# Performance work log

Measured on AMD Instinct MI355X. Metric: run time of the kernel, lower is better.

The kernel has to match this reference:

```python
import jax, jax.numpy as jnp
import numpy as np

N = 50000
TOPK = 32
IN_C = 128
OUT_C = 64
NEG_SLOPE = 0.2
BN_EPS = 1e-5


def setup_inputs() -> dict:
    key = jax.random.key(0)
    ks = jax.random.split(key, 8)
    x = jax.random.normal(ks[0], (N, IN_C), dtype=jnp.float32)
    embedding = jax.random.normal(ks[1], (N, OUT_C), dtype=jnp.float32)
    # edges: each node has TOPK incoming edges, no self loops
    tgt = jnp.repeat(jnp.arange(N, dtype=jnp.int64), TOPK)
    off = jax.random.randint(ks[2], (N * TOPK,), 1, N, dtype=jnp.int64)
    src = (tgt + off) % N
    edge_index = jnp.stack([src, tgt], axis=0)
    lin_w = jax.random.normal(ks[3], (OUT_C, IN_C), dtype=jnp.float32) * (1.0 / np.sqrt(IN_C))
    att_i = jax.random.normal(ks[4], (1, 1, OUT_C), dtype=jnp.float32) * 0.1
    att_j = jax.random.normal(ks[5], (1, 1, OUT_C), dtype=jnp.float32) * 0.1
    att_em_i = jax.random.normal(ks[6], (1, 1, OUT_C), dtype=jnp.float32) * 0.1
    att_em_j = jax.random.normal(ks[7], (1, 1, OUT_C), dtype=jnp.float32) * 0.1
    bias = jnp.zeros((OUT_C,), dtype=jnp.float32)
    bn_gamma = jnp.ones((OUT_C,), dtype=jnp.float32)
    bn_beta = jnp.zeros((OUT_C,), dtype=jnp.float32)
    return {"x": x, "embedding": embedding, "edge_index": edge_index,
            "lin_w": lin_w, "att_i": att_i, "att_j": att_j,
            "att_em_i": att_em_i, "att_em_j": att_em_j, "bias": bias,
            "bn_gamma": bn_gamma, "bn_beta": bn_beta}


def _gnn_forward(x, embedding, lin_w, att_i, att_j, att_em_i, att_em_j,
                 bias, bn_gamma, bn_beta, src, tgt):
    n = x.shape[0]
    # linear transform: [N, heads=1, OUT_C]
    x_lin = (x @ lin_w.T).reshape(n, 1, OUT_C)
    # gather per edge (self loops already appended to src/tgt)
    x_i = x_lin[tgt]                      # [Etot, 1, C]
    x_j = x_lin[src]                      # [Etot, 1, C]
    emb_i = embedding[tgt][:, None, :]    # [Etot, 1, C]
    emb_j = embedding[src][:, None, :]
    # attention logits, eq (6)-(8)
    alpha = ((x_i * att_i).sum(-1) + (emb_i * att_em_i).sum(-1)
             + (x_j * att_j).sum(-1) + (emb_j * att_em_j).sum(-1))  # [Etot, 1]
    alpha = jnp.where(alpha >= 0, alpha, NEG_SLOPE * alpha)
    # segment softmax over incoming edges of each target node
    m = jax.ops.segment_max(alpha, tgt, num_segments=n)
    m = jnp.where(jnp.isfinite(m), m, 0.0)
    e = jnp.exp(alpha - m[tgt])
    denom = jax.ops.segment_sum(e, tgt, num_segments=n)
    alpha = e / (denom[tgt] + 1e-16)      # [Etot, 1]
    # weighted scatter-add aggregation
    msg = x_j * alpha[:, :, None]         # [Etot, 1, C]
    out = jax.ops.segment_sum(msg, tgt, num_segments=n).reshape(n, OUT_C)
    out = out + bias
    # BatchNorm1d (training-mode batch stats, biased var) + ReLU
    mu = out.mean(axis=0)
    var = ((out - mu) ** 2).mean(axis=0)
    out = (out - mu) / jnp.sqrt(var + BN_EPS) * bn_gamma + bn_beta
    return jax.nn.relu(out)


def reference(x, embedding, edge_index, lin_w, att_i, att_j, att_em_i,
              att_em_j, bias, bn_gamma, bn_beta):
    n = x.shape[0]
    loops = jnp.arange(n, dtype=edge_index.dtype)
    src = jnp.concatenate([edge_index[0], loops])
    tgt = jnp.concatenate([edge_index[1], loops])
    return _gnn_forward(x, embedding, lin_w, att_i, att_j, att_em_i,
                        att_em_j, bias, bn_gamma, bn_beta, src, tgt)
```

## Files before the change

kernel.cpp:

```cpp
#include <hip/hip_runtime.h>

#define NN 50000
#define TOPK 32
#define IN_C 128
#define OUT_C 64
#define NEG_SLOPE 0.2f
#define BN_EPS 1e-5f

#define K1_BLOCKS (NN / 16)
#define K2_BLOCKS (NN / 8)

#define WS_XBF   0
#define WS_AI    (NN * 32)
#define WS_AJ    (WS_AI + NN)
#define WS_SUMS  (WS_AJ + NN)

typedef __bf16 bf16x8 __attribute__((ext_vector_type(8)));
typedef float f32x4 __attribute__((ext_vector_type(4)));
union BF8 { unsigned p[4]; bf16x8 v; };

__device__ inline float leaky(float a) { return a >= 0.f ? a : NEG_SLOPE * a; }
__device__ inline float bl(unsigned u) { return __uint_as_float(u << 16); }
__device__ inline float bh(unsigned u) { return __uint_as_float(u & 0xffff0000u); }

__device__ inline unsigned pk2bf(float lo, float hi) {
    union { __bf16 b[2]; unsigned u; } cv;
    cv.b[0] = (__bf16)lo; cv.b[1] = (__bf16)hi;
    return cv.u;
}
__device__ inline unsigned short f2bf(float f) {
    union { __bf16 b; unsigned short u; } cv;
    cv.b = (__bf16)f;
    return cv.u;
}

__device__ inline void async16(const uint4* g, uint4* l) {
    __builtin_amdgcn_global_load_lds(
        (const __attribute__((address_space(1))) void*)(const void*)g,
        (__attribute__((address_space(3))) void*)(void*)l, 16, 0, 0);
}

__global__ __launch_bounds__(256) void k1_mfma(
    const float* __restrict__ x, const float* __restrict__ emb,
    const float* __restrict__ lin_w,
    const float* __restrict__ att_i, const float* __restrict__ att_j,
    const float* __restrict__ att_em_i, const float* __restrict__ att_em_j,
    unsigned short* __restrict__ x_bf, float* __restrict__ a_i,
    float* __restrict__ a_j, float* __restrict__ sums)
{
    __shared__ float redi[16][5], redj[16][5];
    __shared__ float eredi[16][17], eredj[16][17];
    const int tid = threadIdx.x;
    if (blockIdx.x == 0) {
#pragma unroll
        for (int i = 0; i < 4; ++i) sums[tid + i * 256] = 0.f;
    }

    const int lane = tid & 63;
    const int wv = tid >> 6;
    const int quad = lane >> 4;
    const int nn = lane & 15;
    const int base = blockIdx.x * 16;
    const int c = wv * 16 + nn;

    BF8 bfr[4], afr[4];
    {
        const float* wr = lin_w + (size_t)c * IN_C + quad * 8;
        const float* xr = x + (size_t)(base + nn) * IN_C + quad * 8;
#pragma unroll
        for (int s = 0; s < 4; ++s) {
            const float4 wa = *(const float4*)(wr + s * 32);
            const float4 wb = *(const float4*)(wr + s * 32 + 4);
            const float4 xa = *(const float4*)(xr + s * 32);
            const float4 xb = *(const float4*)(xr + s * 32 + 4);
            bfr[s].p[0] = pk2bf(wa.x, wa.y);
            bfr[s].p[1] = pk2bf(wa.z, wa.w);
            bfr[s].p[2] = pk2bf(wb.x, wb.y);
            bfr[s].p[3] = pk2bf(wb.z, wb.w);
            afr[s].p[0] = pk2bf(xa.x, xa.y);
            afr[s].p[1] = pk2bf(xa.z, xa.w);
            afr[s].p[2] = pk2bf(xb.x, xb.y);
            afr[s].p[3] = pk2bf(xb.z, xb.w);
        }
    }

    f32x4 acc = {0.f, 0.f, 0.f, 0.f};
#pragma unroll
    for (int s = 0; s < 4; ++s)
        acc = __builtin_amdgcn_mfma_f32_16x16x32_bf16(afr[s].v, bfr[s].v, acc,
                                                      0, 0, 0);

    const float aic = att_i[c], ajc = att_j[c];
    float pi[4], pj[4];
#pragma unroll
    for (int r = 0; r < 4; ++r) {
        const int node = base + quad * 4 + r;
        x_bf[(size_t)node * OUT_C + c] = f2bf(acc[r]);
        pi[r] = acc[r] * aic;
        pj[r] = acc[r] * ajc;
    }
#pragma unroll
    for (int d = 1; d < 16; d <<= 1) {
#pragma unroll
        for (int r = 0; r < 4; ++r) {
            pi[r] += __shfl_xor(pi[r], d, 64);
            pj[r] += __shfl_xor(pj[r], d, 64);
        }
    }
    if (nn == 0) {
#pragma unroll
        for (int r = 0; r < 4; ++r) {
            redi[quad * 4 + r][wv] = pi[r];
            redj[quad * 4 + r][wv] = pj[r];
        }
    }
    {
        const int nl = tid >> 4, c4 = tid & 15;
        const float4 e4 = ((const float4*)emb)[(size_t)(base + nl) * 16 + c4];
        const float4 i4 = ((const float4*)att_em_i)[c4];
        const float4 j4 = ((const float4*)att_em_j)[c4];
        eredi[nl][c4] = e4.x * i4.x + e4.y * i4.y + e4.z * i4.z + e4.w * i4.w;
        eredj[nl][c4] = e4.x * j4.x + e4.y * j4.y + e4.z * j4.z + e4.w * j4.w;
    }
    __syncthreads();
    if (tid < 16) {
        float si = redi[tid][0] + redi[tid][1] + redi[tid][2] + redi[tid][3];
        float sj = redj[tid][0] + redj[tid][1] + redj[tid][2] + redj[tid][3];
#pragma unroll
        for (int r = 0; r < 16; ++r) { si += eredi[tid][r]; sj += eredj[tid][r]; }
        a_i[base + tid] = si;
        a_j[base + tid] = sj;
    }
}

__global__ __launch_bounds__(64) void k2_attn(
    const int* __restrict__ src, const uint4* __restrict__ x_bf4,
    const float* __restrict__ a_j, const float* __restrict__ a_i,
    const float* __restrict__ bias, float* __restrict__ out,
    float* __restrict__ sums)
{
    __shared__ uint4 stage[33 * 64];
    __shared__ float wbuf[8][36];
    __shared__ float sb1[64][9], sb2[64][9];

    const int tid = threadIdx.x;
    const int g = tid >> 3;
    const int q = tid & 7;
    const int t = blockIdx.x * 8 + g;

    const int4* sp4 = (const int4*)(src + (size_t)t * TOPK);
    int4 s4[8];
#pragma unroll
    for (int i = 0; i < 8; ++i) s4[i] = sp4[i];
    const int4 sq = sp4[q];

#pragma unroll
    for (int i = 0; i < 8; ++i) {
        async16(x_bf4 + ((size_t)s4[i].x * 8 + q), &stage[(i * 4 + 0) * 64]);
        async16(x_bf4 + ((size_t)s4[i].y * 8 + q), &stage[(i * 4 + 1) * 64]);
        async16(x_bf4 + ((size_t)s4[i].z * 8 + q), &stage[(i * 4 + 2) * 64]);
        async16(x_bf4 + ((size_t)s4[i].w * 8 + q), &stage[(i * 4 + 3) * 64]);
    }
    async16(x_bf4 + ((size_t)t * 8 + q), &stage[32 * 64]);

    const float ai_t = a_i[t];
    float l0 = leaky(ai_t + a_j[sq.x]);
    float l1 = leaky(ai_t + a_j[sq.y]);
    float l2 = leaky(ai_t + a_j[sq.z]);
    float l3 = leaky(ai_t + a_j[sq.w]);
    const float ls = leaky(ai_t + a_j[t]);
    float mx = fmaxf(fmaxf(l0, l1), fmaxf(l2, l3));
#pragma unroll
    for (int d = 1; d < 8; d <<= 1) mx = fmaxf(mx, __shfl_xor(mx, d, 64));
    mx = fmaxf(mx, ls);
    const float e0 = __expf(l0 - mx), e1 = __expf(l1 - mx);
    const float e2 = __expf(l2 - mx), e3 = __expf(l3 - mx);
    const float es = __expf(ls - mx);
    float den = (e0 + e1) + (e2 + e3);
#pragma unroll
    for (int d = 1; d < 8; d <<= 1) den += __shfl_xor(den, d, 64);
    den += es + 1e-16f;
    const float inv = 1.f / den;

    ((float4*)&wbuf[g][q * 4])[0] =
        make_float4(e0 * inv, e1 * inv, e2 * inv, e3 * inv);
    if (q == 0) wbuf[g][32] = es * inv;
    __syncthreads();

    float4 w4[8];
#pragma unroll
    for (int i = 0; i < 8; ++i) w4[i] = ((const float4*)wbuf[g])[i];
    const float wself = wbuf[g][32];

    __builtin_amdgcn_s_waitcnt(0x0F70);
    __syncthreads();

    float A[8];
#pragma unroll
    for (int j = 0; j < 8; ++j) A[j] = 0.f;
#pragma unroll
    for (int e = 0; e < 33; ++e) {
        const uint4 u = stage[e * 64 + tid];
        const float w = (e < 32) ? ((const float*)&w4[e >> 2])[e & 3] : wself;
        A[0] = fmaf(w, bl(u.x), A[0]); A[1] = fmaf(w, bh(u.x), A[1]);
        A[2] = fmaf(w, bl(u.y), A[2]); A[3] = fmaf(w, bh(u.y), A[3]);
        A[4] = fmaf(w, bl(u.z), A[4]); A[5] = fmaf(w, bh(u.z), A[5]);
        A[6] = fmaf(w, bl(u.w), A[6]); A[7] = fmaf(w, bh(u.w), A[7]);
    }
    const float4 b0 = ((const float4*)bias)[q * 2];
    const float4 b1 = ((const float4*)bias)[q * 2 + 1];
    float v[8];
    v[0] = A[0] + b0.x; v[1] = A[1] + b0.y; v[2] = A[2] + b0.z; v[3] = A[3] + b0.w;
    v[4] = A[4] + b1.x; v[5] = A[5] + b1.y; v[6] = A[6] + b1.z; v[7] = A[7] + b1.w;
    float4* o4 = (float4*)(out + (size_t)t * OUT_C + q * 8);
    o4[0] = make_float4(v[0], v[1], v[2], v[3]);
    o4[1] = make_float4(v[4], v[5], v[6], v[7]);

#pragma unroll
    for (int j = 0; j < 8; ++j) {
        sb1[q * 8 + j][g] = v[j];
        sb2[q * 8 + j][g] = v[j] * v[j];
    }
    __syncthreads();
    {
        float t1 = 0.f, t2 = 0.f;
#pragma unroll
        for (int r = 0; r < 8; ++r) { t1 += sb1[tid][r]; t2 += sb2[tid][r]; }
        float* rep = sums + (blockIdx.x & 7) * 128;
        atomicAdd(&rep[tid], t1);
        atomicAdd(&rep[64 + tid], t2);
    }
}

__global__ __launch_bounds__(256) void k4_bn(
    float* __restrict__ out, const float* __restrict__ sums,
    const float* __restrict__ gamma, const float* __restrict__ beta)
{
    __shared__ float s_sc[64], s_sh[64];
    const int tid = threadIdx.x;
    if (tid < 64) {
        float s1 = 0.f, s2 = 0.f;
#pragma unroll
        for (int r = 0; r < 8; ++r) {
            s1 += sums[r * 128 + tid];
            s2 += sums[r * 128 + 64 + tid];
        }
        const float mu = s1 / (float)NN;
        const float ex2 = s2 / (float)NN;
        const float var = fmaxf(ex2 - mu * mu, 0.f);
        const float sc = gamma[tid] / sqrtf(var + BN_EPS);
        s_sc[tid] = sc;
        s_sh[tid] = beta[tid] - mu * sc;
    }
    __syncthreads();
    const int total = NN * OUT_C / 4;
    float4* p = (float4*)out;
    for (int idx = blockIdx.x * 256 + tid; idx < total; idx += gridDim.x * 256) {
        float4 v = p[idx];
        const int c0 = (idx & 15) * 4;
        v.x = fmaxf(fmaf(v.x, s_sc[c0 + 0], s_sh[c0 + 0]), 0.f);
        v.y = fmaxf(fmaf(v.y, s_sc[c0 + 1], s_sh[c0 + 1]), 0.f);
        v.z = fmaxf(fmaf(v.z, s_sc[c0 + 2], s_sh[c0 + 2]), 0.f);
        v.w = fmaxf(fmaf(v.w, s_sc[c0 + 3], s_sh[c0 + 3]), 0.f);
        p[idx] = v;
    }
}

extern "C" void kernel_launch(void* const* d_in, const int* in_sizes, int n_in,
                              void* d_out, int out_size, void* d_ws, size_t ws_size,
                              hipStream_t stream) {
    const float* x        = (const float*)d_in[0];
    const float* emb      = (const float*)d_in[1];
    const int*   edge     = (const int*)d_in[2];
    const float* lin_w    = (const float*)d_in[3];
    const float* att_i    = (const float*)d_in[4];
    const float* att_j    = (const float*)d_in[5];
    const float* att_em_i = (const float*)d_in[6];
    const float* att_em_j = (const float*)d_in[7];
    const float* bias     = (const float*)d_in[8];
    const float* gamma    = (const float*)d_in[9];
    const float* beta     = (const float*)d_in[10];

    float* ws    = (float*)d_ws;
    unsigned short* x_bf = (unsigned short*)(ws + WS_XBF);
    float* a_i   = ws + WS_AI;
    float* a_j   = ws + WS_AJ;
    float* sums  = ws + WS_SUMS;
    float* out   = (float*)d_out;

    k1_mfma<<<K1_BLOCKS, 256, 0, stream>>>(x, emb, lin_w, att_i, att_j,
                                           att_em_i, att_em_j, x_bf, a_i, a_j, sums);
    k2_attn<<<K2_BLOCKS, 64, 0, stream>>>(edge, (const uint4*)x_bf, a_j, a_i,
                                          bias, out, sums);
    k4_bn<<<1024, 256, 0, stream>>>(out, sums, gamma, beta);
}
```

Baseline: 164.0 us.

## Make attention kernel persistent over node groups with index prefetch

The per-edge attention/aggregation kernel now launches 1024 blocks, and each block loops over 6-7 consecutive groups of 8 target nodes instead of launching one block per group. While the current group is being reduced, the next group's source indices and attention scalars are loaded early, and the next gather is issued after the stats atomics. The goal is to cut block launch overhead and hide some index-load latency. The cost is no overlap of the x gathers with compute inside a block, since the stage buffer is single, plus an extra barrier per iteration and fewer resident waves for latency hiding.

```diff
diff --git a/kernel.cpp b/kernel.cpp
--- a/kernel.cpp
+++ b/kernel.cpp
@@ -8,7 +8,8 @@
 #define BN_EPS 1e-5f
 
 #define K1_BLOCKS (NN / 16)
-#define K2_BLOCKS (NN / 8)
+#define K2_GROUPS (NN / 8)
+#define K2_BLOCKS 1024
 
 #define WS_XBF   0
 #define WS_AI    (NN * 32)
@@ -146,89 +147,129 @@
     const int tid = threadIdx.x;
     const int g = tid >> 3;
     const int q = tid & 7;
-    const int t = blockIdx.x * 8 + g;
-
-    const int4* sp4 = (const int4*)(src + (size_t)t * TOPK);
-    int4 s4[8];
-#pragma unroll
-    for (int i = 0; i < 8; ++i) s4[i] = sp4[i];
-    const int4 sq = sp4[q];
-
-#pragma unroll
-    for (int i = 0; i < 8; ++i) {
-        async16(x_bf4 + ((size_t)s4[i].x * 8 + q), &stage[(i * 4 + 0) * 64]);
-        async16(x_bf4 + ((size_t)s4[i].y * 8 + q), &stage[(i * 4 + 1) * 64]);
-        async16(x_bf4 + ((size_t)s4[i].z * 8 + q), &stage[(i * 4 + 2) * 64]);
-        async16(x_bf4 + ((size_t)s4[i].w * 8 + q), &stage[(i * 4 + 3) * 64]);
-    }
-    async16(x_bf4 + ((size_t)t * 8 + q), &stage[32 * 64]);
-
-    const float ai_t = a_i[t];
-    float l0 = leaky(ai_t + a_j[sq.x]);
-    float l1 = leaky(ai_t + a_j[sq.y]);
-    float l2 = leaky(ai_t + a_j[sq.z]);
-    float l3 = leaky(ai_t + a_j[sq.w]);
-    const float ls = leaky(ai_t + a_j[t]);
-    float mx = fmaxf(fmaxf(l0, l1), fmaxf(l2, l3));
-#pragma unroll
-    for (int d = 1; d < 8; d <<= 1) mx = fmaxf(mx, __shfl_xor(mx, d, 64));
-    mx = fmaxf(mx, ls);
-    const float e0 = __expf(l0 - mx), e1 = __expf(l1 - mx);
-    const float e2 = __expf(l2 - mx), e3 = __expf(l3 - mx);
-    const float es = __expf(ls - mx);
-    float den = (e0 + e1) + (e2 + e3);
-#pragma unroll
-    for (int d = 1; d < 8; d <<= 1) den += __shfl_xor(den, d, 64);
-    den += es + 1e-16f;
-    const float inv = 1.f / den;
-
-    ((float4*)&wbuf[g][q * 4])[0] =
-        make_float4(e0 * inv, e1 * inv, e2 * inv, e3 * inv);
-    if (q == 0) wbuf[g][32] = es * inv;
-    __syncthreads();
-
-    float4 w4[8];
-#pragma unroll
-    for (int i = 0; i < 8; ++i) w4[i] = ((const float4*)wbuf[g])[i];
-    const float wself = wbuf[g][32];
-
-    __builtin_amdgcn_s_waitcnt(0x0F70);
-    __syncthreads();
-
-    float A[8];
-#pragma unroll
-    for (int j = 0; j < 8; ++j) A[j] = 0.f;
-#pragma unroll
-    for (int e = 0; e < 33; ++e) {
-        const uint4 u = stage[e * 64 + tid];
-        const float w = (e < 32) ? ((const float*)&w4[e >> 2])[e & 3] : wself;
-        A[0] = fmaf(w, bl(u.x), A[0]); A[1] = fmaf(w, bh(u.x), A[1]);
-        A[2] = fmaf(w, bl(u.y), A[2]); A[3] = fmaf(w, bh(u.y), A[3]);
-        A[4] = fmaf(w, bl(u.z), A[4]); A[5] = fmaf(w, bh(u.z), A[5]);
-        A[6] = fmaf(w, bl(u.w), A[6]); A[7] = fmaf(w, bh(u.w), A[7]);
-    }
-    const float4 b0 = ((const float4*)bias)[q * 2];
-    const float4 b1 = ((const float4*)bias)[q * 2 + 1];
-    float v[8];
-    v[0] = A[0] + b0.x; v[1] = A[1] + b0.y; v[2] = A[2] + b0.z; v[3] = A[3] + b0.w;
-    v[4] = A[4] + b1.x; v[5] = A[5] + b1.y; v[6] = A[6] + b1.z; v[7] = A[7] + b1.w;
-    float4* o4 = (float4*)(out + (size_t)t * OUT_C + q * 8);
-    o4[0] = make_float4(v[0], v[1], v[2], v[3]);
-    o4[1] = make_float4(v[4], v[5], v[6], v[7]);
-
-#pragma unroll
-    for (int j = 0; j < 8; ++j) {
-        sb1[q * 8 + j][g] = v[j];
-        sb2[q * 8 + j][g] = v[j] * v[j];
-    }
-    __syncthreads();
+    const int b = blockIdx.x;
+
+    int gi = b * 6 + (b < 106 ? b : 106);
+    const int gend = gi + (b < 106 ? 7 : 6);
+
+    int t = gi * 8 + g;
+
     {
-        float t1 = 0.f, t2 = 0.f;
-#pragma unroll
-        for (int r = 0; r < 8; ++r) { t1 += sb1[tid][r]; t2 += sb2[tid][r]; }
-        float* rep = sums + (blockIdx.x & 7) * 128;
-        atomicAdd(&rep[tid], t1);
-        atomicAdd(&rep[64 + tid], t2);
+        const int4* sp4 = (const int4*)(src + (size_t)t * TOPK);
+        int4 s4[8];
+#pragma unroll
+        for (int i = 0; i < 8; ++i) s4[i] = sp4[i];
+        int4 sq = sp4[q];
+        float ai_t = a_i[t], ajs = a_j[t];
+        float aj0 = a_j[sq.x], aj1 = a_j[sq.y], aj2 = a_j[sq.z], aj3 = a_j[sq.w];
+
+#pragma unroll
+        for (int i = 0; i < 8; ++i) {
+            async16(x_bf4 + ((size_t)s4[i].x * 8 + q), &stage[(i * 4 + 0) * 64]);
+            async16(x_bf4 + ((size_t)s4[i].y * 8 + q), &stage[(i * 4 + 1) * 64]);
+            async16(x_bf4 + ((size_t)s4[i].z * 8 + q), &stage[(i * 4 + 2) * 64]);
+            async16(x_bf4 + ((size_t)s4[i].w * 8 + q), &stage[(i * 4 + 3) * 64]);
+        }
+        async16(x_bf4 + ((size_t)t * 8 + q), &stage[32 * 64]);
+
+        for (;;) {
+            float l0 = leaky(ai_t + aj0);
+            float l1 = leaky(ai_t + aj1);
+            float l2 = leaky(ai_t + aj2);
+            float l3 = leaky(ai_t + aj3);
+            const float ls = leaky(ai_t + ajs);
+            float mx = fmaxf(fmaxf(l0, l1), fmaxf(l2, l3));
+#pragma unroll
+            for (int d = 1; d < 8; d <<= 1) mx = fmaxf(mx, __shfl_xor(mx, d, 64));
+            mx = fmaxf(mx, ls);
+            const float e0 = __expf(l0 - mx), e1 = __expf(l1 - mx);
+            const float e2 = __expf(l2 - mx), e3 = __expf(l3 - mx);
+            const float es = __expf(ls - mx);
+            float den = (e0 + e1) + (e2 + e3);
+#pragma unroll
+            for (int d = 1; d < 8; d <<= 1) den += __shfl_xor(den, d, 64);
+            den += es + 1e-16f;
+            const float inv = 1.f / den;
+
+            ((float4*)&wbuf[g][q * 4])[0] =
+                make_float4(e0 * inv, e1 * inv, e2 * inv, e3 * inv);
+            if (q == 0) wbuf[g][32] = es * inv;
+            __syncthreads();
+
+            float4 w4[8];
+#pragma unroll
+            for (int i = 0; i < 8; ++i) w4[i] = ((const float4*)wbuf[g])[i];
+            const float wself = wbuf[g][32];
+
+            __builtin_amdgcn_s_waitcnt(0x0F70);
+            __syncthreads();
+
+            const bool more = (gi + 1 < gend);
+            const int tn = t + 8;
+            if (more) {
+                const int4* np4 = (const int4*)(src + (size_t)tn * TOPK);
+#pragma unroll
+                for (int i = 0; i < 8; ++i) s4[i] = np4[i];
+                sq   = np4[q];
+                ai_t = a_i[tn];
+                ajs  = a_j[tn];
+            }
+
+            float A[8];
+#pragma unroll
+            for (int j = 0; j < 8; ++j) A[j] = 0.f;
+#pragma unroll
+            for (int e = 0; e < 33; ++e) {
+                const uint4 u = stage[e * 64 + tid];
+                const float w =
+                    (e < 32) ? ((const float*)&w4[e >> 2])[e & 3] : wself;
+                A[0] = fmaf(w, bl(u.x), A[0]); A[1] = fmaf(w, bh(u.x), A[1]);
+                A[2] = fmaf(w, bl(u.y), A[2]); A[3] = fmaf(w, bh(u.y), A[3]);
+                A[4] = fmaf(w, bl(u.z), A[4]); A[5] = fmaf(w, bh(u.z), A[5]);
+                A[6] = fmaf(w, bl(u.w), A[6]); A[7] = fmaf(w, bh(u.w), A[7]);
+            }
+            const float4 b0 = ((const float4*)bias)[q * 2];
+            const float4 b1 = ((const float4*)bias)[q * 2 + 1];
+            float v[8];
+            v[0] = A[0] + b0.x; v[1] = A[1] + b0.y;
+            v[2] = A[2] + b0.z; v[3] = A[3] + b0.w;
+            v[4] = A[4] + b1.x; v[5] = A[5] + b1.y;
+            v[6] = A[6] + b1.z; v[7] = A[7] + b1.w;
+            float4* o4 = (float4*)(out + (size_t)t * OUT_C + q * 8);
+            o4[0] = make_float4(v[0], v[1], v[2], v[3]);
+            o4[1] = make_float4(v[4], v[5], v[6], v[7]);
+
+#pragma unroll
+            for (int j = 0; j < 8; ++j) {
+                sb1[q * 8 + j][g] = v[j];
+                sb2[q * 8 + j][g] = v[j] * v[j];
+            }
+            __syncthreads();
+            {
+                float t1 = 0.f, t2 = 0.f;
+#pragma unroll
+                for (int r = 0; r < 8; ++r) { t1 += sb1[tid][r]; t2 += sb2[tid][r]; }
+                float* rep = sums + (gi & 7) * 128;
+                atomicAdd(&rep[tid], t1);
+                atomicAdd(&rep[64 + tid], t2);
+            }
+
+            if (!more) break;
+
+            __syncthreads();
+            aj0 = a_j[sq.x]; aj1 = a_j[sq.y];
+            aj2 = a_j[sq.z]; aj3 = a_j[sq.w];
+#pragma unroll
+            for (int i = 0; i < 8; ++i) {
+                async16(x_bf4 + ((size_t)s4[i].x * 8 + q), &stage[(i * 4 + 0) * 64]);
+                async16(x_bf4 + ((size_t)s4[i].y * 8 + q), &stage[(i * 4 + 1) * 64]);
+                async16(x_bf4 + ((size_t)s4[i].z * 8 + q), &stage[(i * 4 + 2) * 64]);
+                async16(x_bf4 + ((size_t)s4[i].w * 8 + q), &stage[(i * 4 + 3) * 64]);
+            }
+            async16(x_bf4 + ((size_t)tn * 8 + q), &stage[32 * 64]);
+            t = tn;
+            ++gi;
+        }
     }
 }
 
```

Result: slower. 170.1 us (+3.7%).
